# Performance work log

Hardware: AMD Instinct MI355X
Metric: run time of the kernel (lower is better)

Reference implementation:

```python
import jax, jax.numpy as jnp
import numpy as np
from jax import lax

FPLANE = 64
T = 8          # num_segments
HEADS = 4
EPS = 1e-5


def _conv2d(x, w, b):
    # x: [N,C,H,W], w: [O,I,kh,kw]
    y = lax.conv_general_dilated(x, w, (1, 1), 'SAME',
                                 dimension_numbers=('NCHW', 'OIHW', 'NCHW'))
    return y + b[None, :, None, None]


def _conv3d_grouped(x, w, b, groups):
    # x: [N,C,D,H,W], w: [O, C//groups, kd,kh,kw]
    y = lax.conv_general_dilated(x, w, (1, 1, 1), 'SAME',
                                 dimension_numbers=('NCDHW', 'OIDHW', 'NCDHW'),
                                 feature_group_count=groups)
    return y + b[None, :, None, None, None]


def setup_inputs() -> dict:
    key = jax.random.key(0)
    ks = jax.random.split(key, 5)
    N, C, H, W = T * 16, FPLANE, 56, 56
    x = jax.random.normal(ks[0], (N, C, H, W), dtype=jnp.float32)
    attn_w = jax.random.normal(ks[1], (HEADS, C, 3, 3), dtype=jnp.float32) * 0.05
    attn_b = jax.random.normal(ks[2], (HEADS,), dtype=jnp.float32) * 0.05
    bn_gamma = jnp.ones((C,), dtype=jnp.float32)
    bn_beta = jnp.zeros((C,), dtype=jnp.float32)
    conv3d_w = jax.random.normal(ks[3], (2, C // 2, 3, 3, 3), dtype=jnp.float32) * 0.05
    conv3d_b = jax.random.normal(ks[4], (2,), dtype=jnp.float32) * 0.05
    return {'x': x, 'attn_w': attn_w, 'attn_b': attn_b,
            'bn_gamma': bn_gamma, 'bn_beta': bn_beta,
            'conv3d_w': conv3d_w, 'conv3d_b': conv3d_b}


def reference(x, attn_w, attn_b, bn_gamma, bn_beta, conv3d_w, conv3d_b):
    N, C, H, W = x.shape
    B = N // T
    half = C // 2
    quarter = C // 4

    # spatial attention: conv2d -> ReLU -> Sigmoid, per-head gating
    attn = jax.nn.sigmoid(jax.nn.relu(_conv2d(x, attn_w, attn_b)))  # [N,HEADS,H,W]
    xh = x.reshape(N, HEADS, C // HEADS, H, W) * attn[:, :, None]
    x2 = xh.reshape(N, C, H, W)

    # [B*T,C,H,W] -> [B,C,T,H,W]
    x5 = x2.reshape(B, T, C, H, W).transpose(0, 2, 1, 3, 4)

    # BatchNorm3d (training-mode batch statistics) + ReLU
    mean = jnp.mean(x5, axis=(0, 2, 3, 4), keepdims=True)
    var = jnp.var(x5, axis=(0, 2, 3, 4), keepdims=True)
    x_bn = (x5 - mean) * lax.rsqrt(var + EPS)
    x_bn = x_bn * bn_gamma[None, :, None, None, None] + bn_beta[None, :, None, None, None]
    x_bn_relu = jax.nn.relu(x_bn)

    # grouped conv3d gate (2 groups, 1 output channel each), tanh
    gate = jnp.tanh(_conv3d_grouped(x_bn_relu, conv3d_w, conv3d_b, groups=2))  # [B,2,T,H,W]
    g1 = gate[:, 0:1]
    g2 = gate[:, 1:2]

    x_g1 = x5[:, :half]
    x_g2 = x5[:, half:]
    y1 = g1 * x_g1
    y2 = g2 * x_g2
    r1 = x_g1 - y1
    r2 = x_g2 - y2

    pad_t = ((0, 0), (0, 0), (0, 1), (0, 0), (0, 0))
    pad_b = ((0, 0), (0, 0), (1, 0), (0, 0), (0, 0))
    y1 = jnp.pad(y1[:, :, 1:], pad_t) + r1   # left shift in time, zero pad
    y2 = jnp.pad(y2[:, :, :-1], pad_b) + r2  # right shift in time, zero pad

    # interleave sub-halves: view [B,2,C/4,T,H,W] -> permute -> [B,C/2,T,H,W]
    def interleave(y):
        return (y.reshape(B, 2, quarter, T, H, W)
                 .transpose(0, 2, 1, 3, 4, 5)
                 .reshape(B, half, T, H, W))

    y = jnp.concatenate([interleave(y1), interleave(y2)], axis=1)  # [B,C,T,H,W]
    return y.transpose(0, 2, 1, 3, 4).reshape(N, C, H, W)
```

## Files before the change

kernel.cpp:

```cpp
#include <hip/hip_runtime.h>
#include <hip/hip_bf16.h>

#define HW 3136
#define CTOT 64
#define NTOT 128
#define BB 16
#define TTT 8

static __device__ __forceinline__ float bf2f(unsigned short u) {
    union { unsigned int ui; float f; } v;
    v.ui = ((unsigned int)u) << 16;
    return v.f;
}
static __device__ __forceinline__ unsigned short f2bf(float f) {
    union { float f; unsigned int u; } v;
    v.f = f;
    unsigned int u = v.u;
    unsigned int r = (u + 0x7fffu + ((u >> 16) & 1u)) >> 16;
    return (unsigned short)r;
}

__global__ void k_repack(const float* __restrict__ aw, float* __restrict__ wpk) {
    const int idx = blockIdx.x * 256 + threadIdx.x;
    if (idx >= 2304) return;
    const int hd = idx & 3;
    const int kw = (idx >> 2) % 3;
    const int dh = (idx / 12) % 3;
    const int c = idx / 36;
    wpk[idx] = aw[hd * 576 + c * 9 + dh * 3 + kw];
}

__global__ __launch_bounds__(128) void k_attn(const float* __restrict__ x,
                                              const float* __restrict__ wpk,
                                              const float* __restrict__ ab,
                                              float* __restrict__ attn,
                                              float* __restrict__ stats) {
    const int tile = blockIdx.x % 49;
    const int n = blockIdx.x / 49;
    const int chunk = threadIdx.x >> 4;
    const int qi = threadIdx.x & 15;
    const int quad = tile * 16 + qi;
    const int q = quad % 14;
    const int h = quad / 14;
    const int w0 = q * 4;

    __shared__ float wl[2304];
    __shared__ float l[8][16][17];
    __shared__ float4 abuf[4][16];

    const float* xn = x + (size_t)n * CTOT * HW;
    const int c0 = chunk * 8;

    auto loadrows = [&](int c, float r[3][6]) {
#pragma unroll
        for (int dh = 0; dh < 3; ++dh) {
            const int hh = h + dh - 1;
            const bool v = (hh >= 0) && (hh < 56);
            const float* row = xn + c * HW + (v ? hh : h) * 56 + w0;
            const float m = v ? 1.f : 0.f;
            const float4 mid = *(const float4*)row;
            const float e0 = row[(q > 0) ? -1 : 0] * ((q > 0) ? m : 0.f);
            const float e5 = row[(q < 13) ? 4 : 3] * ((q < 13) ? m : 0.f);
            r[dh][0] = e0;
            r[dh][1] = mid.x * m; r[dh][2] = mid.y * m;
            r[dh][3] = mid.z * m; r[dh][4] = mid.w * m;
            r[dh][5] = e5;
        }
    };

    float bufA[3][6], bufB[3][6];
    loadrows(c0, bufA);

#pragma unroll
    for (int i = 0; i < 18; ++i) wl[threadIdx.x + i * 128] = wpk[threadIdx.x + i * 128];
    __syncthreads();

    float acc[4][4];
#pragma unroll
    for (int hd = 0; hd < 4; ++hd)
#pragma unroll
        for (int j = 0; j < 4; ++j) acc[hd][j] = 0.f;

    float midst[8][4];

#pragma unroll
    for (int i = 0; i < 8; ++i) {
        float (*cur)[6] = (i & 1) ? bufB : bufA;
        float (*nxt)[6] = (i & 1) ? bufA : bufB;
        if (i < 7) loadrows(c0 + i + 1, nxt);

        midst[i][0] = cur[1][1]; midst[i][1] = cur[1][2];
        midst[i][2] = cur[1][3]; midst[i][3] = cur[1][4];

        const int c = c0 + i;
#pragma unroll
        for (int dh = 0; dh < 3; ++dh) {
            const float* wb = &wl[c * 36 + dh * 12];
            const float4 wk0 = *(const float4*)(wb);
            const float4 wk1 = *(const float4*)(wb + 4);
            const float4 wk2 = *(const float4*)(wb + 8);
#pragma unroll
            for (int j = 0; j < 4; ++j) {
                const float a0 = cur[dh][j], a1 = cur[dh][j + 1], a2 = cur[dh][j + 2];
                acc[0][j] = fmaf(a0, wk0.x, fmaf(a1, wk1.x, fmaf(a2, wk2.x, acc[0][j])));
                acc[1][j] = fmaf(a0, wk0.y, fmaf(a1, wk1.y, fmaf(a2, wk2.y, acc[1][j])));
                acc[2][j] = fmaf(a0, wk0.z, fmaf(a1, wk1.z, fmaf(a2, wk2.z, acc[2][j])));
                acc[3][j] = fmaf(a0, wk0.w, fmaf(a1, wk1.w, fmaf(a2, wk2.w, acc[3][j])));
            }
        }
    }

    float* mine = &l[chunk][qi][0];
#pragma unroll
    for (int hd = 0; hd < 4; ++hd)
#pragma unroll
        for (int j = 0; j < 4; ++j) mine[hd * 4 + j] = acc[hd][j];
    __syncthreads();

    if (threadIdx.x < 64) {
        const int hd = threadIdx.x >> 4;
        const int rq = threadIdx.x & 15;
        float s0 = ab[hd], s1 = s0, s2 = s0, s3 = s0;
#pragma unroll
        for (int cch = 0; cch < 8; ++cch) {
            const float* p = &l[cch][rq][hd * 4];
            s0 += p[0]; s1 += p[1]; s2 += p[2]; s3 += p[3];
        }
        float4 o;
        o.x = s0 > 0.f ? 1.f / (1.f + __expf(-s0)) : 0.5f;
        o.y = s1 > 0.f ? 1.f / (1.f + __expf(-s1)) : 0.5f;
        o.z = s2 > 0.f ? 1.f / (1.f + __expf(-s2)) : 0.5f;
        o.w = s3 > 0.f ? 1.f / (1.f + __expf(-s3)) : 0.5f;
        *(float4*)(attn + (size_t)(n * 4 + hd) * HW + (tile * 16 + rq) * 4) = o;
        abuf[hd][rq] = o;
    }
    __syncthreads();

    const int head = chunk >> 1;
    const float4 a4 = abuf[head][qi];
    float s[8], sq[8];
#pragma unroll
    for (int i = 0; i < 8; ++i) {
        const float v0 = midst[i][0] * a4.x;
        const float v1 = midst[i][1] * a4.y;
        const float v2 = midst[i][2] * a4.z;
        const float v3 = midst[i][3] * a4.w;
        s[i] = v0 + v1 + v2 + v3;
        sq[i] = v0 * v0 + v1 * v1 + v2 * v2 + v3 * v3;
    }
#pragma unroll
    for (int i = 0; i < 8; ++i) { mine[i] = s[i]; mine[8 + i] = sq[i]; }
    __syncthreads();
    {
        const int ch2 = threadIdx.x >> 4;
        const int k = threadIdx.x & 15;
        float t = 0.f;
#pragma unroll
        for (int qq = 0; qq < 16; ++qq) t += l[ch2][qq][k];
        const int cc = ch2 * 8 + (k & 7);
        const int rep = blockIdx.x & 15;
        atomicAdd(&stats[rep * 128 + (k >> 3) * 64 + cc], t);
    }
}

__global__ void k_finalize(const float* __restrict__ stats,
                           const float* __restrict__ gamma,
                           const float* __restrict__ beta,
                           float* __restrict__ ss) {
    const int c = threadIdx.x;
    float S = 0.f, Q = 0.f;
#pragma unroll
    for (int r = 0; r < 16; ++r) {
        S += stats[r * 128 + c];
        Q += stats[r * 128 + 64 + c];
    }
    const float cnt = 401408.0f;
    const float mean = S / cnt;
    const float var = Q / cnt - mean * mean;
    const float scale = gamma[c] * rsqrtf(var + 1e-5f);
    ss[c] = scale;
    ss[64 + c] = beta[c] - mean * scale;
}

__global__ __launch_bounds__(256) void k_xbnr(const float* __restrict__ x,
                                              const float* __restrict__ attn,
                                              const float* __restrict__ ss,
                                              unsigned short* __restrict__ xbnr) {
    const int i4 = blockIdx.x * 256 + threadIdx.x;
    const int base = i4 * 4;
    const int plane = base / HW;
    const int i = base - plane * HW;
    const int c = plane & 63;
    const int n = plane >> 6;
    const float4 xv = *(const float4*)(x + (size_t)base);
    const float4 av = *(const float4*)(attn + (size_t)(n * 4 + (c >> 4)) * HW + i);
    const float sc = ss[c], sh = ss[64 + c];
    ushort4 o;
    o.x = f2bf(fmaxf(fmaf(xv.x * av.x, sc, sh), 0.f));
    o.y = f2bf(fmaxf(fmaf(xv.y * av.y, sc, sh), 0.f));
    o.z = f2bf(fmaxf(fmaf(xv.z * av.z, sc, sh), 0.f));
    o.w = f2bf(fmaxf(fmaf(xv.w * av.w, sc, sh), 0.f));
    *(ushort4*)(xbnr + (size_t)base) = o;
}

__global__ __launch_bounds__(128) void k_conv3d(const unsigned short* __restrict__ xbnr,
                                                const float* __restrict__ w3,
                                                const float* __restrict__ b3,
                                                float* __restrict__ gate) {
    const int tile = blockIdx.x % 49;
    const int oc = (blockIdx.x / 49) & 1;
    const int b = blockIdx.x / 98;
    const int chunk = threadIdx.x >> 4;
    const int qi = threadIdx.x & 15;
    const int quad = tile * 16 + qi;
    const int q = quad % 14;
    const int h = quad / 14;
    const int w0 = q * 4;

    float acc[8][4];
#pragma unroll
    for (int t = 0; t < 8; ++t)
#pragma unroll
        for (int j = 0; j < 4; ++j) acc[t][j] = 0.f;

    const int ic0 = chunk * 4;
    for (int ic = ic0; ic < ic0 + 4; ++ic) {
        const int c = oc * 32 + ic;
        const unsigned short* cbase = xbnr + (size_t)(b * 8 * 64 + c) * HW;
        const float* wic = w3 + (oc * 32 + ic) * 27;
#pragma unroll
        for (int tt = 0; tt < 8; ++tt) {
            const unsigned short* plane = cbase + (size_t)tt * (64 * HW);
#pragma unroll
            for (int dh = 0; dh < 3; ++dh) {
                const int hh = h + dh - 1;
                if (hh < 0 || hh >= 56) continue;
                const unsigned short* row = plane + hh * 56 + w0;
                const ushort4 mid = *(const ushort4*)row;
                const float f0 = (q > 0) ? bf2f(row[-1]) : 0.f;
                const float f1 = bf2f(mid.x), f2 = bf2f(mid.y);
                const float f3 = bf2f(mid.z), f4 = bf2f(mid.w);
                const float f5 = (q < 13) ? bf2f(row[4]) : 0.f;
#pragma unroll
                for (int dt = 0; dt < 3; ++dt) {
                    const int t = tt + 1 - dt;
                    if (t < 0 || t > 7) continue;
                    const float* wp = wic + dt * 9 + dh * 3;
                    const float wa = wp[0], wb = wp[1], wc = wp[2];
                    acc[t][0] = fmaf(f0, wa, fmaf(f1, wb, fmaf(f2, wc, acc[t][0])));
                    acc[t][1] = fmaf(f1, wa, fmaf(f2, wb, fmaf(f3, wc, acc[t][1])));
                    acc[t][2] = fmaf(f2, wa, fmaf(f3, wb, fmaf(f4, wc, acc[t][2])));
                    acc[t][3] = fmaf(f3, wa, fmaf(f4, wb, fmaf(f5, wc, acc[t][3])));
                }
            }
        }
    }

    __shared__ float4 l4[8 * 16 * 9];
    float4* mine = &l4[(chunk * 16 + qi) * 9];
#pragma unroll
    for (int t = 0; t < 8; ++t) {
        float4 v;
        v.x = acc[t][0]; v.y = acc[t][1]; v.z = acc[t][2]; v.w = acc[t][3];
        mine[t] = v;
    }
    __syncthreads();

    const int rt = threadIdx.x >> 4;
    const int rq = threadIdx.x & 15;
    float4 s = l4[(0 * 16 + rq) * 9 + rt];
#pragma unroll
    for (int c = 1; c < 8; ++c) {
        const float4 v = l4[(c * 16 + rq) * 9 + rt];
        s.x += v.x; s.y += v.y; s.z += v.z; s.w += v.w;
    }
    const float bb = b3[oc];
    float4 o;
    o.x = tanhf(s.x + bb);
    o.y = tanhf(s.y + bb);
    o.z = tanhf(s.z + bb);
    o.w = tanhf(s.w + bb);
    const int outquad = tile * 16 + rq;
    *(float4*)(gate + (size_t)((b * 2 + oc) * 8 + rt) * HW + outquad * 4) = o;
}

__global__ __launch_bounds__(256) void k_final(const float* __restrict__ x,
                                               const float* __restrict__ attn,
                                               const float* __restrict__ gate,
                                               float* __restrict__ out) {
    const int gt = blockIdx.x * 256 + threadIdx.x;
    const int q = gt % 14;
    int r = gt / 14;
    const int h = r % 56;
    r /= 56;
    const int co = r & 63;
    const int b = r >> 6;
    const int sp = h * 56 + q * 4;

    int cs, grp;
    if (co < 32) {
        cs = ((co & 1) << 4) | (co >> 1);
        grp = 0;
    } else {
        const int cc = co - 32;
        cs = 32 + (((cc & 1) << 4) | (cc >> 1));
        grp = 1;
    }
    const int head = cs >> 4;

    float4 x2[8], g[8];
#pragma unroll
    for (int t = 0; t < 8; ++t) {
        const int n = b * 8 + t;
        const float4 xv = *(const float4*)(x + (size_t)(n * 64 + cs) * HW + sp);
        const float4 av = *(const float4*)(attn + (size_t)(n * 4 + head) * HW + sp);
        const float4 gv = *(const float4*)(gate + (size_t)((b * 2 + grp) * 8 + t) * HW + sp);
        x2[t].x = xv.x * av.x;
        x2[t].y = xv.y * av.y;
        x2[t].z = xv.z * av.z;
        x2[t].w = xv.w * av.w;
        g[t] = gv;
    }
#pragma unroll
    for (int t = 0; t < 8; ++t) {
        float4 o;
        o.x = x2[t].x * (1.f - g[t].x);
        o.y = x2[t].y * (1.f - g[t].y);
        o.z = x2[t].z * (1.f - g[t].z);
        o.w = x2[t].w * (1.f - g[t].w);
        if (grp == 0) {
            if (t < 7) {
                o.x += x2[t + 1].x * g[t + 1].x;
                o.y += x2[t + 1].y * g[t + 1].y;
                o.z += x2[t + 1].z * g[t + 1].z;
                o.w += x2[t + 1].w * g[t + 1].w;
            }
        } else {
            if (t > 0) {
                o.x += x2[t - 1].x * g[t - 1].x;
                o.y += x2[t - 1].y * g[t - 1].y;
                o.z += x2[t - 1].z * g[t - 1].z;
                o.w += x2[t - 1].w * g[t - 1].w;
            }
        }
        *(float4*)(out + (size_t)((b * 8 + t) * 64 + co) * HW + sp) = o;
    }
}

extern "C" void kernel_launch(void* const* d_in, const int* in_sizes, int n_in,
                              void* d_out, int out_size, void* d_ws, size_t ws_size,
                              hipStream_t stream) {
    const float* x = (const float*)d_in[0];
    const float* aw = (const float*)d_in[1];
    const float* ab = (const float*)d_in[2];
    const float* gamma = (const float*)d_in[3];
    const float* beta = (const float*)d_in[4];
    const float* w3 = (const float*)d_in[5];
    const float* b3 = (const float*)d_in[6];
    float* out = (float*)d_out;

    char* ws = (char*)d_ws;
    unsigned short* xbnr = (unsigned short*)ws;
    float* attn = (float*)(ws + 51380224);
    float* gate = (float*)(ws + 57802752);
    float* stats = (float*)(ws + 57802752);
    float* ss = (float*)(ws + 61014528);
    float* wpk = (float*)(ws + 61015040);

    hipMemsetAsync(stats, 0, 8192, stream);
    k_repack<<<9, 256, 0, stream>>>(aw, wpk);
    k_attn<<<6272, 128, 0, stream>>>(x, wpk, ab, attn, stats);
    k_finalize<<<1, 64, 0, stream>>>(stats, gamma, beta, ss);
    k_xbnr<<<25088, 256, 0, stream>>>(x, attn, ss, xbnr);
    k_conv3d<<<1568, 128, 0, stream>>>(xbnr, w3, b3, gate);
    k_final<<<3136, 256, 0, stream>>>(x, attn, gate, out);
}
```

Measured before the change: 372.8 us.

## Fuse BN-apply into conv3d and emit attention-gated bf16 activations from attn kernel

The attention kernel now writes the attention-gated activations as bf16 directly, and the separate BN+ReLU pass (k_xbnr) is removed. The conv3d kernel applies the BN scale/shift and ReLU on the fly while loading, with branch-free masked halo loads. The weight repack kernel is folded into the attn kernel's shared-memory load, and k_final is relaunched with 448-thread blocks mapped per row and channel group. This removes one full read of x plus attn and two kernel launches, in exchange for redundant BN arithmetic inside the conv3d inner loop and a larger store in k_attn.

```diff
diff --git a/kernel.cpp b/kernel.cpp
--- a/kernel.cpp
+++ b/kernel.cpp
@@ -20,20 +20,11 @@
     return (unsigned short)r;
 }
 
-__global__ void k_repack(const float* __restrict__ aw, float* __restrict__ wpk) {
-    const int idx = blockIdx.x * 256 + threadIdx.x;
-    if (idx >= 2304) return;
-    const int hd = idx & 3;
-    const int kw = (idx >> 2) % 3;
-    const int dh = (idx / 12) % 3;
-    const int c = idx / 36;
-    wpk[idx] = aw[hd * 576 + c * 9 + dh * 3 + kw];
-}
-
 __global__ __launch_bounds__(128) void k_attn(const float* __restrict__ x,
-                                              const float* __restrict__ wpk,
+                                              const float* __restrict__ aw,
                                               const float* __restrict__ ab,
                                               float* __restrict__ attn,
+                                              unsigned short* __restrict__ x2,
                                               float* __restrict__ stats) {
     const int tile = blockIdx.x % 49;
     const int n = blockIdx.x / 49;
@@ -72,7 +63,14 @@
     loadrows(c0, bufA);
 
 #pragma unroll
-    for (int i = 0; i < 18; ++i) wl[threadIdx.x + i * 128] = wpk[threadIdx.x + i * 128];
+    for (int i = 0; i < 18; ++i) {
+        const int idx = threadIdx.x + i * 128;
+        const int hd = idx & 3;
+        const int kw = (idx >> 2) % 3;
+        const int dh = (idx / 12) % 3;
+        const int c = idx / 36;
+        wl[idx] = aw[hd * 576 + c * 9 + dh * 3 + kw];
+    }
     __syncthreads();
 
     float acc[4][4];
@@ -145,6 +143,9 @@
         const float v1 = midst[i][1] * a4.y;
         const float v2 = midst[i][2] * a4.z;
         const float v3 = midst[i][3] * a4.w;
+        ushort4 o;
+        o.x = f2bf(v0); o.y = f2bf(v1); o.z = f2bf(v2); o.w = f2bf(v3);
+        *(ushort4*)(x2 + (size_t)(n * 64 + c0 + i) * HW + quad * 4) = o;
         s[i] = v0 + v1 + v2 + v3;
         sq[i] = v0 * v0 + v1 * v1 + v2 * v2 + v3 * v3;
     }
@@ -182,28 +183,8 @@
     ss[64 + c] = beta[c] - mean * scale;
 }
 
-__global__ __launch_bounds__(256) void k_xbnr(const float* __restrict__ x,
-                                              const float* __restrict__ attn,
-                                              const float* __restrict__ ss,
-                                              unsigned short* __restrict__ xbnr) {
-    const int i4 = blockIdx.x * 256 + threadIdx.x;
-    const int base = i4 * 4;
-    const int plane = base / HW;
-    const int i = base - plane * HW;
-    const int c = plane & 63;
-    const int n = plane >> 6;
-    const float4 xv = *(const float4*)(x + (size_t)base);
-    const float4 av = *(const float4*)(attn + (size_t)(n * 4 + (c >> 4)) * HW + i);
-    const float sc = ss[c], sh = ss[64 + c];
-    ushort4 o;
-    o.x = f2bf(fmaxf(fmaf(xv.x * av.x, sc, sh), 0.f));
-    o.y = f2bf(fmaxf(fmaf(xv.y * av.y, sc, sh), 0.f));
-    o.z = f2bf(fmaxf(fmaf(xv.z * av.z, sc, sh), 0.f));
-    o.w = f2bf(fmaxf(fmaf(xv.w * av.w, sc, sh), 0.f));
-    *(ushort4*)(xbnr + (size_t)base) = o;
-}
-
-__global__ __launch_bounds__(128) void k_conv3d(const unsigned short* __restrict__ xbnr,
+__global__ __launch_bounds__(128) void k_conv3d(const unsigned short* __restrict__ x2,
+                                                const float* __restrict__ ss,
                                                 const float* __restrict__ w3,
                                                 const float* __restrict__ b3,
                                                 float* __restrict__ gate) {
@@ -226,31 +207,43 @@
     const int ic0 = chunk * 4;
     for (int ic = ic0; ic < ic0 + 4; ++ic) {
         const int c = oc * 32 + ic;
-        const unsigned short* cbase = xbnr + (size_t)(b * 8 * 64 + c) * HW;
-        const float* wic = w3 + (oc * 32 + ic) * 27;
+        const float sc = ss[c], sh = ss[64 + c];
+        const unsigned short* cbase = x2 + (size_t)(b * 8 * 64 + c) * HW;
+        const float* wic = w3 + c * 27;
 #pragma unroll
         for (int tt = 0; tt < 8; ++tt) {
             const unsigned short* plane = cbase + (size_t)tt * (64 * HW);
+            float f[3][6];
 #pragma unroll
             for (int dh = 0; dh < 3; ++dh) {
                 const int hh = h + dh - 1;
-                if (hh < 0 || hh >= 56) continue;
-                const unsigned short* row = plane + hh * 56 + w0;
+                const bool vld = (hh >= 0) && (hh < 56);
+                const unsigned short* row = plane + (vld ? hh : h) * 56 + w0;
+                const float m = vld ? 1.f : 0.f;
+                const float mL = (q > 0) ? m : 0.f;
+                const float mR = (q < 13) ? m : 0.f;
                 const ushort4 mid = *(const ushort4*)row;
-                const float f0 = (q > 0) ? bf2f(row[-1]) : 0.f;
-                const float f1 = bf2f(mid.x), f2 = bf2f(mid.y);
-                const float f3 = bf2f(mid.z), f4 = bf2f(mid.w);
-                const float f5 = (q < 13) ? bf2f(row[4]) : 0.f;
+                const unsigned short e0 = row[(q > 0) ? -1 : 0];
+                const unsigned short e5 = row[(q < 13) ? 4 : 3];
+                f[dh][0] = fmaxf(fmaf(bf2f(e0),    sc, sh), 0.f) * mL;
+                f[dh][1] = fmaxf(fmaf(bf2f(mid.x), sc, sh), 0.f) * m;
+                f[dh][2] = fmaxf(fmaf(bf2f(mid.y), sc, sh), 0.f) * m;
+                f[dh][3] = fmaxf(fmaf(bf2f(mid.z), sc, sh), 0.f) * m;
+                f[dh][4] = fmaxf(fmaf(bf2f(mid.w), sc, sh), 0.f) * m;
+                f[dh][5] = fmaxf(fmaf(bf2f(e5),    sc, sh), 0.f) * mR;
+            }
+#pragma unroll
+            for (int dh = 0; dh < 3; ++dh) {
 #pragma unroll
                 for (int dt = 0; dt < 3; ++dt) {
                     const int t = tt + 1 - dt;
                     if (t < 0 || t > 7) continue;
                     const float* wp = wic + dt * 9 + dh * 3;
                     const float wa = wp[0], wb = wp[1], wc = wp[2];
-                    acc[t][0] = fmaf(f0, wa, fmaf(f1, wb, fmaf(f2, wc, acc[t][0])));
-                    acc[t][1] = fmaf(f1, wa, fmaf(f2, wb, fmaf(f3, wc, acc[t][1])));
-                    acc[t][2] = fmaf(f2, wa, fmaf(f3, wb, fmaf(f4, wc, acc[t][2])));
-                    acc[t][3] = fmaf(f3, wa, fmaf(f4, wb, fmaf(f5, wc, acc[t][3])));
+                    acc[t][0] = fmaf(f[dh][0], wa, fmaf(f[dh][1], wb, fmaf(f[dh][2], wc, acc[t][0])));
+                    acc[t][1] = fmaf(f[dh][1], wa, fmaf(f[dh][2], wb, fmaf(f[dh][3], wc, acc[t][1])));
+                    acc[t][2] = fmaf(f[dh][2], wa, fmaf(f[dh][3], wb, fmaf(f[dh][4], wc, acc[t][2])));
+                    acc[t][3] = fmaf(f[dh][3], wa, fmaf(f[dh][4], wb, fmaf(f[dh][5], wc, acc[t][3])));
                 }
             }
         }
@@ -284,63 +277,61 @@
     *(float4*)(gate + (size_t)((b * 2 + oc) * 8 + rt) * HW + outquad * 4) = o;
 }
 
-__global__ __launch_bounds__(256) void k_final(const float* __restrict__ x,
+__global__ __launch_bounds__(448) void k_final(const float* __restrict__ x,
                                                const float* __restrict__ attn,
                                                const float* __restrict__ gate,
                                                float* __restrict__ out) {
-    const int gt = blockIdx.x * 256 + threadIdx.x;
-    const int q = gt % 14;
-    int r = gt / 14;
-    const int h = r % 56;
-    r /= 56;
-    const int co = r & 63;
-    const int b = r >> 6;
+    const int hg = blockIdx.x & 1;
+    const int h = (blockIdx.x >> 1) % 56;
+    const int b = blockIdx.x / 112;
+    const int q = threadIdx.x % 14;
+    const int col = threadIdx.x / 14;
+    const int co = hg * 32 + col;
     const int sp = h * 56 + q * 4;
 
-    int cs, grp;
+    int cs;
     if (co < 32) {
         cs = ((co & 1) << 4) | (co >> 1);
-        grp = 0;
     } else {
         const int cc = co - 32;
         cs = 32 + (((cc & 1) << 4) | (cc >> 1));
-        grp = 1;
-    }
+    }
+    const int grp = hg;
     const int head = cs >> 4;
 
-    float4 x2[8], g[8];
+    float4 x2v[8], g[8];
 #pragma unroll
     for (int t = 0; t < 8; ++t) {
         const int n = b * 8 + t;
         const float4 xv = *(const float4*)(x + (size_t)(n * 64 + cs) * HW + sp);
         const float4 av = *(const float4*)(attn + (size_t)(n * 4 + head) * HW + sp);
         const float4 gv = *(const float4*)(gate + (size_t)((b * 2 + grp) * 8 + t) * HW + sp);
-        x2[t].x = xv.x * av.x;
-        x2[t].y = xv.y * av.y;
-        x2[t].z = xv.z * av.z;
-        x2[t].w = xv.w * av.w;
+        x2v[t].x = xv.x * av.x;
+        x2v[t].y = xv.y * av.y;
+        x2v[t].z = xv.z * av.z;
+        x2v[t].w = xv.w * av.w;
         g[t] = gv;
     }
 #pragma unroll
     for (int t = 0; t < 8; ++t) {
         float4 o;
-        o.x = x2[t].x * (1.f - g[t].x);
-        o.y = x2[t].y * (1.f - g[t].y);
-        o.z = x2[t].z * (1.f - g[t].z);
-        o.w = x2[t].w * (1.f - g[t].w);
+        o.x = x2v[t].x * (1.f - g[t].x);
+        o.y = x2v[t].y * (1.f - g[t].y);
+        o.z = x2v[t].z * (1.f - g[t].z);
+        o.w = x2v[t].w * (1.f - g[t].w);
         if (grp == 0) {
             if (t < 7) {
-                o.x += x2[t + 1].x * g[t + 1].x;
-                o.y += x2[t + 1].y * g[t + 1].y;
-                o.z += x2[t + 1].z * g[t + 1].z;
-                o.w += x2[t + 1].w * g[t + 1].w;
+                o.x += x2v[t + 1].x * g[t + 1].x;
+                o.y += x2v[t + 1].y * g[t + 1].y;
+                o.z += x2v[t + 1].z * g[t + 1].z;
+                o.w += x2v[t + 1].w * g[t + 1].w;
             }
         } else {
             if (t > 0) {
-                o.x += x2[t - 1].x * g[t - 1].x;
-                o.y += x2[t - 1].y * g[t - 1].y;
-                o.z += x2[t - 1].z * g[t - 1].z;
-                o.w += x2[t - 1].w * g[t - 1].w;
+                o.x += x2v[t - 1].x * g[t - 1].x;
+                o.y += x2v[t - 1].y * g[t - 1].y;
+                o.z += x2v[t - 1].z * g[t - 1].z;
+                o.w += x2v[t - 1].w * g[t - 1].w;
             }
         }
         *(float4*)(out + (size_t)((b * 8 + t) * 64 + co) * HW + sp) = o;
@@ -360,18 +351,15 @@
     float* out = (float*)d_out;
 
     char* ws = (char*)d_ws;
-    unsigned short* xbnr = (unsigned short*)ws;
+    unsigned short* x2 = (unsigned short*)ws;
     float* attn = (float*)(ws + 51380224);
     float* gate = (float*)(ws + 57802752);
     float* stats = (float*)(ws + 57802752);
     float* ss = (float*)(ws + 61014528);
-    float* wpk = (float*)(ws + 61015040);
 
     hipMemsetAsync(stats, 0, 8192, stream);
-    k_repack<<<9, 256, 0, stream>>>(aw, wpk);
-    k_attn<<<6272, 128, 0, stream>>>(x, wpk, ab, attn, stats);
+    k_attn<<<6272, 128, 0, stream>>>(x, aw, ab, attn, x2, stats);
     k_finalize<<<1, 64, 0, stream>>>(stats, gamma, beta, ss);
-    k_xbnr<<<25088, 256, 0, stream>>>(x, attn, ss, xbnr);
-    k_conv3d<<<1568, 128, 0, stream>>>(xbnr, w3, b3, gate);
-    k_final<<<3136, 256, 0, stream>>>(x, attn, gate, out);
-}
+    k_conv3d<<<1568, 128, 0, stream>>>(x2, ss, w3, b3, gate);
+    k_final<<<1792, 448, 0, stream>>>(x, attn, gate, out);
+}
```

New measurement: 391.8 us. 5.1% more time.
